# Optimization experiments

Measured on AMD Instinct MI355X. Metric: run time of the kernel, lower is better.

Reference implementation:

```python
import jax, jax.numpy as jnp
import numpy as np

NEG_INF = -9e15  # matches torch's -9000000000000000.0 fill
ALPHA = 0.2      # LeakyReLU negative slope


def setup_inputs() -> dict:
    key = jax.random.key(0)
    k1, k2, k3, k4 = jax.random.split(key, 4)
    B, F, N, T, C = 16, 128, 256, 64, 64
    h = jax.random.normal(k1, (B, F, N, T), dtype=jnp.float32)
    adj = jax.random.randint(k2, (B, N, N), 0, 2, dtype=jnp.int32)
    W = jax.random.normal(k3, (B, F, C), dtype=jnp.float32)
    a = jax.random.normal(k4, (B, 2 * C, 1), dtype=jnp.float32)
    return {"h": h, "adj": adj, "W": W, "a": a}


def reference(h, adj, W, a):
    # Wh: (B, C, N, T)
    Wh = jnp.einsum('bfnt,bfc->bcnt', h, W)
    C = W.shape[-1]
    # The original builds the O(N^2) pairwise concat then contracts with a.
    # Equivalently: e[b,i,j,t] = leakyrelu(a1.Wh[:, i] + a2.Wh[:, j])
    a1 = a[:, :C, 0]   # (B, C)
    a2 = a[:, C:, 0]   # (B, C)
    f = jnp.einsum('bcnt,bc->bnt', Wh, a1)  # (B, N, T)
    g = jnp.einsum('bcnt,bc->bnt', Wh, a2)  # (B, N, T)
    e = jax.nn.leaky_relu(f[:, :, None, :] + g[:, None, :, :], negative_slope=ALPHA)  # (B,N,N,T)
    mask = adj[:, :, :, None] > 0  # (B, N, N, 1) broadcast over T
    e = jnp.where(mask, e, NEG_INF)
    attention = jax.nn.softmax(e, axis=2)  # softmax over neighbor index m
    # dropout = 0.0 (eval-mode reference), so skipped
    h_prime = jnp.einsum('bnmt,bcmt->bcnt', attention, Wh)
    return jax.nn.elu(h_prime)  # concat=True branch
```

## Files before the change

### kernel.cpp

```cpp
#include <hip/hip_runtime.h>

#define B_ 16
#define F_ 128
#define N_ 256
#define T_ 64
#define C_ 64
#define NEG_INF_ -9000000000000000.0f
#define ALPHA_ 0.2f

typedef short bf16x8 __attribute__((ext_vector_type(8)));
typedef float f32x4 __attribute__((ext_vector_type(4)));

__device__ __forceinline__ unsigned short f2bf(float x){
  unsigned int u = __float_as_uint(x);
  unsigned int r = u + 0x7FFFu + ((u >> 16) & 1u);
  return (unsigned short)(r >> 16);
}
__device__ __forceinline__ unsigned pk2(float a, float b){
  return ((unsigned)f2bf(b) << 16) | (unsigned)f2bf(a);
}

__global__ void k_u(const float* __restrict__ W, const float* __restrict__ a,
                    float* __restrict__ u){
  int b = blockIdx.x, f = threadIdx.x;
  const float* Wb = W + (b*F_ + f)*C_;
  const float* ab = a + b*2*C_;
  float s1 = 0.f, s2 = 0.f;
#pragma unroll 8
  for (int c = 0; c < C_; ++c){
    float w = Wb[c];
    s1 = fmaf(w, ab[c], s1);
    s2 = fmaf(w, ab[C_ + c], s2);
  }
  u[b*F_ + f] = s1;
  u[B_*F_ + b*F_ + f] = s2;
}

__global__ void k_mask(const int* __restrict__ adj, unsigned* __restrict__ amask){
  int blk = blockIdx.x;
  int b = blk >> 2, r0 = (blk & 3)*64;
  int w = threadIdx.x >> 6, l = threadIdx.x & 63;
  const int* ab = adj + ((size_t)b*N_ + r0 + w*16)*N_;
  unsigned* om = amask + ((size_t)b*N_ + r0 + w*16)*8;
  for (int r = 0; r < 16; ++r){
    unsigned long long m0 = __ballot(ab[r*N_ +       l] > 0);
    unsigned long long m1 = __ballot(ab[r*N_ +  64 + l] > 0);
    unsigned long long m2 = __ballot(ab[r*N_ + 128 + l] > 0);
    unsigned long long m3 = __ballot(ab[r*N_ + 192 + l] > 0);
    if (l == 0){
      *(uint4*)(om + r*8)     = make_uint4((unsigned)m0, (unsigned)(m0>>32),
                                           (unsigned)m1, (unsigned)(m1>>32));
      *(uint4*)(om + r*8 + 4) = make_uint4((unsigned)m2, (unsigned)(m2>>32),
                                           (unsigned)m3, (unsigned)(m3>>32));
    }
  }
}

__global__ __launch_bounds__(256, 4) void k_wh(const float* __restrict__ h,
    const float* __restrict__ W, const float* __restrict__ u,
    unsigned short* __restrict__ wht, float* __restrict__ fvec,
    float* __restrict__ gvec){
  __shared__ uint4 hT4[1024];
  __shared__ uint4 wT4[1024];
  __shared__ float fpart[4][T_];
  __shared__ float gpart[4][T_];
  char* hT = (char*)hT4;
  char* wT = (char*)wT4;

  int bid = blockIdx.x, b = bid >> 8, n = bid & 255;
  int tid = threadIdx.x, w = tid >> 6, l = tid & 63;
  const float* hg = h + (size_t)b*F_*N_*T_ + n*T_;
  const float* Wg = W + b*F_*C_;
  const float* u1 = u + b*F_;
  const float* u2 = u + B_*F_ + b*F_;

  float sf = 0.f, sg = 0.f;
#pragma unroll
  for (int p = 0; p < 4; ++p){
    int f0 = p*32 + w*8;
    float v[8], wv[8];
#pragma unroll
    for (int j = 0; j < 8; ++j){
      v[j]  = hg[(size_t)(f0+j)*(N_*T_) + l];
      wv[j] = Wg[(f0+j)*C_ + l];
      sf = fmaf(v[j], u1[f0+j], sf);
      sg = fmaf(v[j], u2[f0+j], sg);
    }
    uint4 ph = make_uint4(pk2(v[0],v[1]),  pk2(v[2],v[3]),  pk2(v[4],v[5]),  pk2(v[6],v[7]));
    uint4 pw = make_uint4(pk2(wv[0],wv[1]),pk2(wv[2],wv[3]),pk2(wv[4],wv[5]),pk2(wv[6],wv[7]));
    *(uint4*)(hT + ((l*256 + f0*2) ^ ((l & 7) << 4))) = ph;
    *(uint4*)(wT + ((l*256 + f0*2) ^ ((l & 7) << 4))) = pw;
  }
  fpart[w][l] = sf;
  gpart[w][l] = sg;
  __syncthreads();

  if (tid < T_){
    float f_ = (fpart[0][tid] + fpart[1][tid]) + (fpart[2][tid] + fpart[3][tid]);
    float g_ = (gpart[0][tid] + gpart[1][tid]) + (gpart[2][tid] + gpart[3][tid]);
    fvec[(b*N_ + n)*T_ + tid] = f_;
    gvec[(b*N_ + n)*T_ + tid] = g_;
  }

  int li = l & 15, g_ = l >> 4;
  bf16x8 afr[4];
#pragma unroll
  for (int ch = 0; ch < 4; ++ch){
    int c = w*16 + li;
    afr[ch] = *(bf16x8*)(wT + ((c*256 + (ch*32 + g_*8)*2) ^ ((c & 7) << 4)));
  }
  f32x4 acc[4];
#pragma unroll
  for (int tt = 0; tt < 4; ++tt) acc[tt] = (f32x4){0.f,0.f,0.f,0.f};
#pragma unroll
  for (int tt = 0; tt < 4; ++tt){
#pragma unroll
    for (int ch = 0; ch < 4; ++ch){
      int t = tt*16 + li;
      bf16x8 bfr = *(bf16x8*)(hT + ((t*256 + (ch*32 + g_*8)*2) ^ ((t & 7) << 4)));
      acc[tt] = __builtin_amdgcn_mfma_f32_16x16x32_bf16(afr[ch], bfr, acc[tt], 0, 0, 0);
    }
  }
  unsigned short* wb = wht + ((size_t)b*T_*N_ + n)*C_;
#pragma unroll
  for (int tt = 0; tt < 4; ++tt){
    int t = tt*16 + li;
    int c0 = w*16 + g_*4;
    unsigned q0 = pk2(acc[tt][0], acc[tt][1]);
    unsigned q1 = pk2(acc[tt][2], acc[tt][3]);
    *(uint2*)(wb + (size_t)t*(N_*C_) + c0) = make_uint2(q0, q1);
  }
}

__global__ __launch_bounds__(256, 3) void k_attn(
    unsigned short* wht,
    const unsigned* __restrict__ amask,
    const float* __restrict__ fvec, const float* __restrict__ gvec){
  __shared__ uint4 whsT4[2048];
  __shared__ uint4 alds4[1024];
  __shared__ float gs[N_];
  __shared__ float invs[N_];
  char* dstT = (char*)whsT4;
  char* aldsb = (char*)alds4;

  int bid = blockIdx.x;
  int b = bid >> 6, t = bid & 63;
  int tid = threadIdx.x, w = tid >> 6, l = tid & 63;

  gs[tid] = gvec[(b*N_ + tid)*T_ + t];
  float fl = fvec[(b*N_ + tid)*T_ + t];
  const unsigned* gmask = amask + ((size_t)b*N_ + tid)*8;
  const uint4* mq = (const uint4*)gmask;
  uint4 mwA = mq[0], mwB = mq[1];

  const char* src = (const char*)(wht + (size_t)(b*T_ + t)*(N_*C_));
#pragma unroll
  for (int i = 0; i < 4; ++i){
    int q2 = tid + i*256;
    int m = (q2 >> 3)*2, c0 = (q2 & 7)*8;
    uint4 ra = *(const uint4*)(src + m*128 + c0*2);
    uint4 rb = *(const uint4*)(src + (m+1)*128 + c0*2);
    unsigned va[4] = {ra.x, ra.y, ra.z, ra.w};
    unsigned vb[4] = {rb.x, rb.y, rb.z, rb.w};
#pragma unroll
    for (int k = 0; k < 4; ++k){
      int c = c0 + 2*k;
      unsigned lo = __builtin_amdgcn_perm(vb[k], va[k], 0x05040100u);
      unsigned hi = __builtin_amdgcn_perm(vb[k], va[k], 0x07060302u);
      *(unsigned*)(dstT + ((( c   *512) + m*2) ^ (((c  ) & 7) << 4))) = lo;
      *(unsigned*)(dstT + ((((c+1)*512) + m*2) ^ (((c+1) & 7) << 4))) = hi;
    }
  }
  __syncthreads();

  float mg = -1e5f;
  {
    unsigned mw[8] = {mwA.x, mwA.y, mwA.z, mwA.w, mwB.x, mwB.y, mwB.z, mwB.w};
#pragma unroll
    for (int i = 0; i < 8; ++i){
      unsigned wd = mw[i];
#pragma unroll
      for (int j4 = 0; j4 < 8; ++j4){
        float4 g4 = *(const float4*)&gs[i*32 + j4*4];
        float s0 = ((wd >> (j4*4+0)) & 1u) ? g4.x : -1e5f;
        float s1 = ((wd >> (j4*4+1)) & 1u) ? g4.y : -1e5f;
        float s2 = ((wd >> (j4*4+2)) & 1u) ? g4.z : -1e5f;
        float s3 = ((wd >> (j4*4+3)) & 1u) ? g4.w : -1e5f;
        mg = fmaxf(mg, fmaxf(fmaxf(s0, s1), fmaxf(s2, s3)));
      }
    }
  }
  float me = fl + mg;
  me = fmaxf(me, ALPHA_*me);

  f32x4 acc[4][4];
#pragma unroll
  for (int mt = 0; mt < 4; ++mt)
#pragma unroll
    for (int nt = 0; nt < 4; ++nt)
      acc[mt][nt] = (f32x4){0.f, 0.f, 0.f, 0.f};
  float sum = 0.f;
  char* aw = aldsb + w*4096;
  int g_ = l >> 4, li = l & 15;

#pragma unroll 1
  for (int ch = 0; ch < 8; ++ch){
    unsigned wd = gmask[ch];
#pragma unroll
    for (int part = 0; part < 4; ++part){
      float4 ga = *(const float4*)&gs[ch*32 + part*8];
      float4 gb = *(const float4*)&gs[ch*32 + part*8 + 4];
      float gg[8] = {ga.x, ga.y, ga.z, ga.w, gb.x, gb.y, gb.z, gb.w};
      float wv[8];
#pragma unroll
      for (int jj = 0; jj < 8; ++jj){
        float e  = fl + gg[jj];
        float lr = fmaxf(e, ALPHA_*e);
        float x  = fminf(lr - me, 0.f);
        float p  = __expf(x);
        float bitf = (float)((wd >> (part*8 + jj)) & 1u);
        float v  = p * bitf;
        sum += v;
        wv[jj] = v;
      }
      unsigned q0 = (__float_as_uint(wv[1]) & 0xFFFF0000u) | (__float_as_uint(wv[0]) >> 16);
      unsigned q1 = (__float_as_uint(wv[3]) & 0xFFFF0000u) | (__float_as_uint(wv[2]) >> 16);
      unsigned q2 = (__float_as_uint(wv[5]) & 0xFFFF0000u) | (__float_as_uint(wv[4]) >> 16);
      unsigned q3 = (__float_as_uint(wv[7]) & 0xFFFF0000u) | (__float_as_uint(wv[6]) >> 16);
      *(uint4*)(aw + ((l*64 + part*16) ^ ((l & 7) << 4))) = make_uint4(q0, q1, q2, q3);
    }
    bf16x8 bfr[4];
#pragma unroll
    for (int nt = 0; nt < 4; ++nt){
      int c = nt*16 + li;
      bfr[nt] = *(bf16x8*)(dstT + ((c*512 + (ch*32 + g_*8)*2) ^ ((c & 7) << 4)));
    }
#pragma unroll
    for (int mt = 0; mt < 4; ++mt){
      int r = mt*16 + li;
      bf16x8 af = *(bf16x8*)(aw + ((r*64 + g_*16) ^ ((r & 7) << 4)));
#pragma unroll
      for (int nt = 0; nt < 4; ++nt)
        acc[mt][nt] = __builtin_amdgcn_mfma_f32_16x16x32_bf16(af, bfr[nt], acc[mt][nt], 0, 0, 0);
    }
  }

  invs[tid] = 1.0f / sum;
  unsigned short* ob = wht + (size_t)(b*T_ + t)*(N_*C_) + (size_t)w*64*C_;
#pragma unroll
  for (int mt = 0; mt < 4; ++mt){
#pragma unroll
    for (int reg = 0; reg < 4; ++reg){
      int row = mt*16 + g_*4 + reg;
      float inv = invs[w*64 + row];
#pragma unroll
      for (int nt = 0; nt < 4; ++nt){
        float v = acc[mt][nt][reg] * inv;
        v = v > 0.f ? v : (__expf(v) - 1.f);
        ob[row*C_ + nt*16 + li] = f2bf(v);
      }
    }
  }
}

__global__ __launch_bounds__(256) void k_tr(const unsigned short* __restrict__ whtO,
                                            float* __restrict__ out){
  __shared__ float tile[64][65];
  int bid = blockIdx.x;
  int b = bid >> 8, n = bid & 255;
  int tid = threadIdx.x;
  const unsigned short* src = whtO + ((size_t)b*T_*N_ + n)*C_;
#pragma unroll
  for (int i = 0; i < 2; ++i){
    int idx = tid + i*256;
    int t = idx >> 3, c0 = (idx & 7)*8;
    uint4 v = *(const uint4*)(src + (size_t)t*(N_*C_) + c0);
    unsigned arr[4] = {v.x, v.y, v.z, v.w};
#pragma unroll
    for (int k = 0; k < 4; ++k){
      tile[c0+2*k  ][t] = __uint_as_float(arr[k] << 16);
      tile[c0+2*k+1][t] = __uint_as_float(arr[k] & 0xFFFF0000u);
    }
  }
  __syncthreads();
  float* ob = out + (size_t)b*C_*N_*T_ + n*T_;
#pragma unroll
  for (int i = 0; i < 4; ++i){
    int idx = tid + i*256;
    int c = idx >> 4, t0 = (idx & 15)*4;
    float4 v = make_float4(tile[c][t0], tile[c][t0+1], tile[c][t0+2], tile[c][t0+3]);
    *(float4*)(ob + (size_t)c*(N_*T_) + t0) = v;
  }
}

extern "C" void kernel_launch(void* const* d_in, const int* in_sizes, int n_in,
                              void* d_out, int out_size, void* d_ws, size_t ws_size,
                              hipStream_t stream){
  (void)in_sizes; (void)n_in; (void)out_size; (void)ws_size;
  const float* h   = (const float*)d_in[0];
  const int*   adj = (const int*)d_in[1];
  const float* W   = (const float*)d_in[2];
  const float* a   = (const float*)d_in[3];
  float* u    = (float*)d_ws;
  float* fvec = u + 2*B_*F_;
  float* gvec = fvec + B_*N_*T_;
  unsigned short* wht = (unsigned short*)(gvec + B_*N_*T_);
  unsigned* amask = (unsigned*)(wht + (size_t)B_*T_*N_*C_);

  k_u   <<<dim3(B_),      dim3(F_),  0, stream>>>(W, a, u);
  k_mask<<<dim3(B_*4),    dim3(256), 0, stream>>>(adj, amask);
  k_wh  <<<dim3(B_*N_),   dim3(256), 0, stream>>>(h, W, u, wht, fvec, gvec);
  k_attn<<<dim3(B_*T_),   dim3(256), 0, stream>>>(wht, amask, fvec, gvec);
  k_tr  <<<dim3(B_*N_),   dim3(256), 0, stream>>>(wht, (float*)d_out);
}
```

Measured before the change: 113.8 us.

## Compute attention weights directly in MFMA A-fragment layout, drop LDS staging

The attention kernel now has each lane compute softmax numerators for the exact rows and columns it feeds into the MFMA A operand, so the per-warp LDS buffer and its write/read round-trip go away. The f/g vectors are pre-scaled by log2(e) and stored transposed so exp2f can be used and loads are contiguous. Masking uses sign-extended bit masks and packing uses v_cvt_pk_bf16_f32, and row max and row sum are reduced with cross-lane shuffles. The freed LDS lets occupancy rise to 4 blocks per CU, at the cost of some redundant exp work and more global reads of mask words.

```diff
diff --git a/kernel.cpp b/kernel.cpp
--- a/kernel.cpp
+++ b/kernel.cpp
@@ -5,8 +5,8 @@
 #define N_ 256
 #define T_ 64
 #define C_ 64
-#define NEG_INF_ -9000000000000000.0f
 #define ALPHA_ 0.2f
+#define L2E_ 1.4426950408889634f
 
 typedef short bf16x8 __attribute__((ext_vector_type(8)));
 typedef float f32x4 __attribute__((ext_vector_type(4)));
@@ -18,6 +18,9 @@
 }
 __device__ __forceinline__ unsigned pk2(float a, float b){
   return ((unsigned)f2bf(b) << 16) | (unsigned)f2bf(a);
+}
+__device__ __forceinline__ unsigned sbit(unsigned w, int j){
+  return (unsigned)(((int)(w << (31 - j))) >> 31);
 }
 
 __global__ void k_u(const float* __restrict__ W, const float* __restrict__ a,
@@ -98,8 +101,8 @@
   if (tid < T_){
     float f_ = (fpart[0][tid] + fpart[1][tid]) + (fpart[2][tid] + fpart[3][tid]);
     float g_ = (gpart[0][tid] + gpart[1][tid]) + (gpart[2][tid] + gpart[3][tid]);
-    fvec[(b*N_ + n)*T_ + tid] = f_;
-    gvec[(b*N_ + n)*T_ + tid] = g_;
+    fvec[(b*T_ + tid)*N_ + n] = f_ * L2E_;
+    gvec[(b*T_ + tid)*N_ + n] = g_ * L2E_;
   }
 
   int li = l & 15, g_ = l >> 4;
@@ -132,26 +135,27 @@
   }
 }
 
-__global__ __launch_bounds__(256, 3) void k_attn(
+__global__ __launch_bounds__(256, 4) void k_attn(
     unsigned short* wht,
     const unsigned* __restrict__ amask,
-    const float* __restrict__ fvec, const float* __restrict__ gvec){
+    const float* __restrict__ fvec,
+    const float* __restrict__ gvec){
   __shared__ uint4 whsT4[2048];
-  __shared__ uint4 alds4[1024];
   __shared__ float gs[N_];
   __shared__ float invs[N_];
   char* dstT = (char*)whsT4;
-  char* aldsb = (char*)alds4;
 
   int bid = blockIdx.x;
   int b = bid >> 6, t = bid & 63;
   int tid = threadIdx.x, w = tid >> 6, l = tid & 63;
-
-  gs[tid] = gvec[(b*N_ + tid)*T_ + t];
-  float fl = fvec[(b*N_ + tid)*T_ + t];
-  const unsigned* gmask = amask + ((size_t)b*N_ + tid)*8;
-  const uint4* mq = (const uint4*)gmask;
-  uint4 mwA = mq[0], mwB = mq[1];
+  int li = l & 15, g_ = l >> 4;
+
+  const float* gp = gvec + (size_t)(b*T_ + t)*N_;
+  const float* fp = fvec + (size_t)(b*T_ + t)*N_;
+  if (tid < 64){
+    float4 gg4 = *(const float4*)(gp + tid*4);
+    *(float4*)&gs[tid*4] = gg4;
+  }
 
   const char* src = (const char*)(wht + (size_t)(b*T_ + t)*(N_*C_));
 #pragma unroll
@@ -173,25 +177,40 @@
   }
   __syncthreads();
 
-  float mg = -1e5f;
-  {
-    unsigned mw[8] = {mwA.x, mwA.y, mwA.z, mwA.w, mwB.x, mwB.y, mwB.z, mwB.w};
-#pragma unroll
-    for (int i = 0; i < 8; ++i){
-      unsigned wd = mw[i];
-#pragma unroll
-      for (int j4 = 0; j4 < 8; ++j4){
-        float4 g4 = *(const float4*)&gs[i*32 + j4*4];
-        float s0 = ((wd >> (j4*4+0)) & 1u) ? g4.x : -1e5f;
-        float s1 = ((wd >> (j4*4+1)) & 1u) ? g4.y : -1e5f;
-        float s2 = ((wd >> (j4*4+2)) & 1u) ? g4.z : -1e5f;
-        float s3 = ((wd >> (j4*4+3)) & 1u) ? g4.w : -1e5f;
-        mg = fmaxf(mg, fmaxf(fmaxf(s0, s1), fmaxf(s2, s3)));
+  const unsigned* mbase = amask + ((size_t)b*N_ + w*64 + li)*8;
+
+  float fl2[4];
+#pragma unroll
+  for (int mt = 0; mt < 4; ++mt) fl2[mt] = fp[w*64 + mt*16 + li];
+
+  float mg2[4] = {-1e30f, -1e30f, -1e30f, -1e30f};
+#pragma unroll 1
+  for (int ch = 0; ch < 8; ++ch){
+    const float* gq = &gs[ch*32 + g_*8];
+    float4 ga = *(const float4*)gq;
+    float4 gb = *(const float4*)(gq + 4);
+    float gg[8] = {ga.x, ga.y, ga.z, ga.w, gb.x, gb.y, gb.z, gb.w};
+#pragma unroll
+    for (int mt = 0; mt < 4; ++mt){
+      unsigned wds = mbase[mt*128 + ch] >> (g_*8);
+#pragma unroll
+      for (int j = 0; j < 8; ++j){
+        float cand = __uint_as_float(__float_as_uint(gg[j]) & sbit(wds, j));
+        mg2[mt] = fmaxf(mg2[mt], cand);
       }
     }
   }
-  float me = fl + mg;
-  me = fmaxf(me, ALPHA_*me);
+  float fme[4], fme2[4];
+#pragma unroll
+  for (int mt = 0; mt < 4; ++mt){
+    float v = mg2[mt];
+    v = fmaxf(v, __shfl_xor(v, 16));
+    v = fmaxf(v, __shfl_xor(v, 32));
+    float em  = fl2[mt] + v;
+    float me2 = fmaxf(em, ALPHA_*em);
+    fme[mt]  = fl2[mt] - me2;
+    fme2[mt] = fmaf(fl2[mt], ALPHA_, -me2);
+  }
 
   f32x4 acc[4][4];
 #pragma unroll
@@ -199,53 +218,54 @@
 #pragma unroll
     for (int nt = 0; nt < 4; ++nt)
       acc[mt][nt] = (f32x4){0.f, 0.f, 0.f, 0.f};
-  float sum = 0.f;
-  char* aw = aldsb + w*4096;
-  int g_ = l >> 4, li = l & 15;
+  float sums[4] = {0.f, 0.f, 0.f, 0.f};
 
 #pragma unroll 1
   for (int ch = 0; ch < 8; ++ch){
-    unsigned wd = gmask[ch];
-#pragma unroll
-    for (int part = 0; part < 4; ++part){
-      float4 ga = *(const float4*)&gs[ch*32 + part*8];
-      float4 gb = *(const float4*)&gs[ch*32 + part*8 + 4];
-      float gg[8] = {ga.x, ga.y, ga.z, ga.w, gb.x, gb.y, gb.z, gb.w};
-      float wv[8];
-#pragma unroll
-      for (int jj = 0; jj < 8; ++jj){
-        float e  = fl + gg[jj];
-        float lr = fmaxf(e, ALPHA_*e);
-        float x  = fminf(lr - me, 0.f);
-        float p  = __expf(x);
-        float bitf = (float)((wd >> (part*8 + jj)) & 1u);
-        float v  = p * bitf;
-        sum += v;
-        wv[jj] = v;
-      }
-      unsigned q0 = (__float_as_uint(wv[1]) & 0xFFFF0000u) | (__float_as_uint(wv[0]) >> 16);
-      unsigned q1 = (__float_as_uint(wv[3]) & 0xFFFF0000u) | (__float_as_uint(wv[2]) >> 16);
-      unsigned q2 = (__float_as_uint(wv[5]) & 0xFFFF0000u) | (__float_as_uint(wv[4]) >> 16);
-      unsigned q3 = (__float_as_uint(wv[7]) & 0xFFFF0000u) | (__float_as_uint(wv[6]) >> 16);
-      *(uint4*)(aw + ((l*64 + part*16) ^ ((l & 7) << 4))) = make_uint4(q0, q1, q2, q3);
-    }
     bf16x8 bfr[4];
 #pragma unroll
     for (int nt = 0; nt < 4; ++nt){
       int c = nt*16 + li;
       bfr[nt] = *(bf16x8*)(dstT + ((c*512 + (ch*32 + g_*8)*2) ^ ((c & 7) << 4)));
     }
+    const float* gq = &gs[ch*32 + g_*8];
+    float4 ga = *(const float4*)gq;
+    float4 gb = *(const float4*)(gq + 4);
+    float gg[8] = {ga.x, ga.y, ga.z, ga.w, gb.x, gb.y, gb.z, gb.w};
 #pragma unroll
     for (int mt = 0; mt < 4; ++mt){
-      int r = mt*16 + li;
-      bf16x8 af = *(bf16x8*)(aw + ((r*64 + g_*16) ^ ((r & 7) << 4)));
+      unsigned wds = mbase[mt*128 + ch] >> (g_*8);
+      float wv[8];
+#pragma unroll
+      for (int j = 0; j < 8; ++j){
+        float d1 = gg[j] + fme[mt];
+        float d2 = fmaf(gg[j], ALPHA_, fme2[mt]);
+        float p  = exp2f(fmaxf(d1, d2));
+        float v  = __uint_as_float(__float_as_uint(p) & sbit(wds, j));
+        sums[mt] += v;
+        wv[j] = v;
+      }
+      unsigned pk0, pk1, pk2_, pk3;
+      asm("v_cvt_pk_bf16_f32 %0, %1, %2" : "=v"(pk0)  : "v"(wv[0]), "v"(wv[1]));
+      asm("v_cvt_pk_bf16_f32 %0, %1, %2" : "=v"(pk1)  : "v"(wv[2]), "v"(wv[3]));
+      asm("v_cvt_pk_bf16_f32 %0, %1, %2" : "=v"(pk2_) : "v"(wv[4]), "v"(wv[5]));
+      asm("v_cvt_pk_bf16_f32 %0, %1, %2" : "=v"(pk3)  : "v"(wv[6]), "v"(wv[7]));
+      union { unsigned u[4]; bf16x8 v; } afu;
+      afu.u[0] = pk0; afu.u[1] = pk1; afu.u[2] = pk2_; afu.u[3] = pk3;
 #pragma unroll
       for (int nt = 0; nt < 4; ++nt)
-        acc[mt][nt] = __builtin_amdgcn_mfma_f32_16x16x32_bf16(af, bfr[nt], acc[mt][nt], 0, 0, 0);
-    }
-  }
-
-  invs[tid] = 1.0f / sum;
+        acc[mt][nt] = __builtin_amdgcn_mfma_f32_16x16x32_bf16(afu.v, bfr[nt], acc[mt][nt], 0, 0, 0);
+    }
+  }
+
+#pragma unroll
+  for (int mt = 0; mt < 4; ++mt){
+    float s = sums[mt];
+    s += __shfl_xor(s, 16);
+    s += __shfl_xor(s, 32);
+    if (g_ == 0) invs[w*64 + mt*16 + li] = 1.0f / s;
+  }
+
   unsigned short* ob = wht + (size_t)(b*T_ + t)*(N_*C_) + (size_t)w*64*C_;
 #pragma unroll
   for (int mt = 0; mt < 4; ++mt){
```

New measurement: 126.6 us. 11.3% more time.
